# Performance work log

Hardware: AMD Instinct MI355X
Metric: run time of the kernel (lower is better)

Reference implementation:

```python
import jax, jax.numpy as jnp
import numpy as np

N, P, M, NCLS = 32, 24564, 32, 81
NEG_POS_RATIO, ALPHA, THRESHOLD = 3, 1.0, 0.5
BACKGROUND = NCLS  # sentinel label for background priors (== n_classes, as in original)


def _rand_boxes(key, prefix):
    # valid normalized xyxy boxes (x2>x1, y2>y1, inside [0,1])
    k1, k2 = jax.random.split(key)
    cxy = jax.random.uniform(k1, prefix + (2,), minval=0.1, maxval=0.9)
    wh = jax.random.uniform(k2, prefix + (2,), minval=0.02, maxval=0.2)
    return jnp.concatenate([cxy - wh / 2, cxy + wh / 2], axis=-1)


def setup_inputs() -> dict:
    key = jax.random.key(0)
    ks = jax.random.split(key, 6)
    return {
        "predicted_boxes": jax.random.normal(ks[0], (N, P, 4), jnp.float32),
        "predicted_class_dist": jax.random.normal(ks[1], (N, P, NCLS), jnp.float32),
        "predicted_objectness": jax.random.uniform(ks[2], (N, P), jnp.float32),
        "anchor_priors": _rand_boxes(ks[3], (P,)),
        "boxes": _rand_boxes(ks[4], (N, M)),
        "labels": jax.random.randint(ks[5], (N, M), 0, NCLS),
    }


def xy_to_cxcy(xy):
    return jnp.concatenate([(xy[..., :2] + xy[..., 2:]) / 2, xy[..., 2:] - xy[..., :2]], axis=-1)


def cxcy_to_gcxgcy(cxcy, priors_cxcy):
    return jnp.concatenate([
        (cxcy[..., :2] - priors_cxcy[..., :2]) / (priors_cxcy[..., 2:] / 10.0),
        jnp.log(cxcy[..., 2:] / priors_cxcy[..., 2:]) * 5.0,
    ], axis=-1)


def box_iou(a, b):  # a: (M,4), b: (P,4) -> (M,P)
    lt = jnp.maximum(a[:, None, :2], b[None, :, :2])
    rb = jnp.minimum(a[:, None, 2:], b[None, :, 2:])
    wh = jnp.clip(rb - lt, 0.0)
    inter = wh[..., 0] * wh[..., 1]
    area_a = (a[:, 2] - a[:, 0]) * (a[:, 3] - a[:, 1])
    area_b = (b[:, 2] - b[:, 0]) * (b[:, 3] - b[:, 1])
    return inter / (area_a[:, None] + area_b[None, :] - inter)


def _match(boxes_i, labels_i, priors):
    # per-image anchor matching (vmapped over batch)
    iou = box_iou(boxes_i, priors)                     # (M, P)
    iou_per_prior = iou.max(axis=0)                    # (P,)
    obj_per_prior = iou.argmax(axis=0)                 # (P,)
    prior_per_obj = iou.argmax(axis=1)                 # (M,)
    obj_per_prior = obj_per_prior.at[prior_per_obj].set(jnp.arange(M))
    iou_per_prior = iou_per_prior.at[prior_per_obj].set(1.0)
    label_per_prior = labels_i[obj_per_prior]
    label_per_prior = jnp.where(iou_per_prior < THRESHOLD, BACKGROUND, label_per_prior)
    true_locs = cxcy_to_gcxgcy(xy_to_cxcy(boxes_i[obj_per_prior]), xy_to_cxcy(priors))
    return true_locs, label_per_prior


def reference(predicted_boxes, predicted_class_dist, predicted_objectness, anchor_priors, boxes, labels):
    true_locs, true_classes = jax.vmap(_match, in_axes=(0, 0, None))(boxes, labels, anchor_priors)
    pos = true_classes != BACKGROUND                   # (N, P) bool
    n_pos_total = pos.sum().astype(jnp.float32)
    posf = pos.astype(jnp.float32)

    # smooth L1 over positive priors (mean over selected elements)
    diff = predicted_boxes - true_locs
    ad = jnp.abs(diff)
    sl1 = jnp.where(ad < 1.0, 0.5 * diff * diff, ad - 0.5)
    loc_loss = jnp.sum(sl1 * posf[..., None]) / (n_pos_total * 4.0)

    # cross entropy over positive priors (mean)
    logp = jax.nn.log_softmax(predicted_class_dist, axis=-1)
    safe_cls = jnp.where(pos, true_classes, 0)
    ce = -jnp.take_along_axis(logp, safe_cls[..., None], axis=-1)[..., 0]
    class_loss_pos = jnp.sum(ce * posf) / n_pos_total

    # objectness MSE: positive mean + hard-negative mining
    obj_loss = (predicted_objectness - posf) ** 2      # (N, P)
    obj_loss_pos = jnp.sum(obj_loss * posf) / n_pos_total

    neg_loss = jnp.where(pos, 0.0, obj_loss)
    neg_sorted = -jnp.sort(-neg_loss, axis=1)          # descending per row
    n_hard = NEG_POS_RATIO * pos.sum(axis=1)           # (N,)
    hmask = (jnp.arange(P)[None, :] < n_hard[:, None]).astype(jnp.float32)
    obj_loss_hardneg = jnp.sum(neg_sorted * hmask) / jnp.maximum(hmask.sum(), 1.0)

    return class_loss_pos + obj_loss_pos + obj_loss_hardneg + ALPHA * loc_loss
```

## Files before the change

kernel.cpp:

```cpp
#include <hip/hip_runtime.h>
#include <math.h>

#define NB 32
#define PP 24564
#define MM 32
#define NCLS 81
#define CHUNK 1024
#define MBLK 24
#define PPW 768
#define BSH 18
#define HB 4096
#define CAPL 2048

#define WS_DONE   0
#define WS_PCNT   32
#define WS_IACC   160
#define WS_PACC   672
#define WS_CPART  9888
#define WS_BKEYP  12960
#define WS_POSBIT 209568
#define WS_M8     307872
#define WS_VAL    1093936

__device__ __forceinline__ float sl1(float d) {
    float a = fabsf(d);
    return a < 1.0f ? 0.5f * d * d : a - 0.5f;
}
__device__ __forceinline__ unsigned long long u64max(unsigned long long a, unsigned long long b) {
    return a > b ? a : b;
}
__device__ __forceinline__ float locv(const float4& pd, const float4& pb,
                                      float gx1, float gy1, float gx2, float gy2) {
    float pcx = (pb.x + pb.z) * 0.5f, pcy = (pb.y + pb.w) * 0.5f;
    float pw = pb.z - pb.x, ph = pb.w - pb.y;
    float g0 = ((gx1 + gx2) * 0.5f - pcx) / (pw / 10.0f);
    float g1 = ((gy1 + gy2) * 0.5f - pcy) / (ph / 10.0f);
    float g2 = logf((gx2 - gx1) / pw) * 5.0f;
    float g3 = logf((gy2 - gy1) / ph) * 5.0f;
    return sl1(pd.x - g0) + sl1(pd.y - g1) + sl1(pd.z - g2) + sl1(pd.w - g3);
}

extern "C" __global__ void __launch_bounds__(256) k_match(
    const float* __restrict__ priors,
    const float* __restrict__ boxes,
    const float* __restrict__ obj,
    const float* __restrict__ pred_boxes,
    const float* __restrict__ pred_cls,
    const int* __restrict__ labels,
    unsigned long long* __restrict__ bkeyp,
    unsigned int* __restrict__ posbit,
    unsigned char* __restrict__ m8,
    float* __restrict__ val,
    int* __restrict__ cpart,
    float* __restrict__ pacc,
    int* __restrict__ done)
{
    const int n = blockIdx.y;
    const int t = threadIdx.x;
    const int lane = t & 63;
    const int wave = t >> 6;
    const int bx = blockIdx.x;
    const int p0 = bx * CHUNK;

    if (bx == 0 && n == 0 && t == 0) *done = 0;

    __shared__ float4 spri[CHUNK];
    __shared__ unsigned char sm8[CHUNK];
    __shared__ float bx0[MM], by0[MM], bx1[MM], by1[MM], bar_[MM];
    __shared__ unsigned long long wk[4][MM];
    __shared__ int bcnt;
    __shared__ float sacc[3];

    float ov[4];
#pragma unroll
    for (int i = 0; i < 4; i++) {
        int p = p0 + t + i * 256;
        float4 v;
        if (p < PP) { v = *(const float4*)(priors + (size_t)p * 4);
                      ov[i] = obj[(size_t)n * PP + p]; }
        else { v.x = 3.f; v.y = 3.f; v.z = 3.5f; v.w = 3.5f; ov[i] = 0.f; }
        spri[t + i * 256] = v;
    }
    if (t < MM) {
        const float* b = boxes + ((size_t)n * MM + t) * 4;
        float x1 = b[0], y1 = b[1], x2 = b[2], y2 = b[3];
        bx0[t] = x1; by0[t] = y1; bx1[t] = x2; by1[t] = y2;
        bar_[t] = (x2 - x1) * (y2 - y1);
    }
    if (t == 0) bcnt = 0;
    if (t < 3) sacc[t] = 0.f;
    __syncthreads();

    float4 pr0 = spri[t], pr1 = spri[t + 256], pr2 = spri[t + 512], pr3 = spri[t + 768];
    const float pa0 = (pr0.z - pr0.x) * (pr0.w - pr0.y);
    const float pa1 = (pr1.z - pr1.x) * (pr1.w - pr1.y);
    const float pa2 = (pr2.z - pr2.x) * (pr2.w - pr2.y);
    const float pa3 = (pr3.z - pr3.x) * (pr3.w - pr3.y);
    unsigned pb0 = 0, pb1 = 0, pb2 = 0, pb3 = 0;

#define DO_IOU(PR, PA, PB, ROFF) { \
        float w = fminf(x1, PR.z) - fmaxf(x0, PR.x); \
        float h = fminf(y1, PR.w) - fmaxf(y0, PR.y); \
        w = fmaxf(w, 0.0f); h = fmaxf(h, 0.0f); \
        float inter = w * h; \
        float iou = inter / (ar + PA - inter); \
        unsigned ib = __float_as_uint(iou); \
        unsigned nk = (ib & 0xFFFFFFE0u) | (unsigned)(31 - m); \
        PB = PB > nk ? PB : nk; \
        unsigned long long kk = ((unsigned long long)ib << 32) \
            | (unsigned long long)(0xFFFFFFFFu - (unsigned)(p0 + t + (ROFF))); \
        km = u64max(km, kk); }

#pragma unroll 2
    for (int m = 0; m < MM; m++) {
        const float x0 = bx0[m], y0 = by0[m], x1 = bx1[m], y1 = by1[m], ar = bar_[m];
        unsigned long long km = 0ULL;
        DO_IOU(pr0, pa0, pb0, 0)
        DO_IOU(pr1, pa1, pb1, 256)
        DO_IOU(pr2, pa2, pb2, 512)
        DO_IOU(pr3, pa3, pb3, 768)
#pragma unroll
        for (int d = 1; d < 64; d <<= 1)
            km = u64max(km, (unsigned long long)__shfl_xor(km, d));
        if (lane == 0) wk[wave][m] = km;
    }
#undef DO_IOU

    int cnt = 0;
    unsigned long long bl[4];
#define ROWOUT(PB, R) { \
        int p = p0 + t + (R) * 256; \
        bool pos = (PB >= 0x3F000000u) && (p < PP); \
        unsigned long long ball = __ballot(pos); \
        bl[R] = ball; \
        unsigned char mb = (unsigned char)(31u - (PB & 31u)); \
        sm8[t + (R) * 256] = mb; \
        if (lane == 0) { \
            int wi = n * PPW + ((p0 + (R) * 256 + wave * 64) >> 5); \
            posbit[wi] = (unsigned)ball; posbit[wi + 1] = (unsigned)(ball >> 32); \
            cnt += __popcll(ball); \
        } \
        if (p < PP) { \
            size_t idx = (size_t)n * PP + p; \
            m8[idx] = mb; \
            val[idx] = pos ? 0.f : ov[R] * ov[R]; \
        } }
    ROWOUT(pb0, 0) ROWOUT(pb1, 1) ROWOUT(pb2, 2) ROWOUT(pb3, 3)
#undef ROWOUT
    if (lane == 0 && cnt) atomicAdd(&bcnt, cnt);

    {
        const int half = lane >> 5, hl = lane & 31;
        float ce_s = 0.f, loc_s = 0.f, op_s = 0.f;
#pragma unroll
        for (int R = 0; R < 4; R++) {
            unsigned long long mask = bl[R];
            const int roff = R * 256 + wave * 64;
            while (mask) {
                int i1 = __ffsll((long long)mask) - 1; mask &= mask - 1;
                int i2 = -1;
                if (mask) { i2 = __ffsll((long long)mask) - 1; mask &= mask - 1; }
                const int pi = half ? i2 : i1;
                const bool act = pi >= 0;
                const int poff = roff + (act ? pi : 0);
                const size_t idx = (size_t)n * PP + p0 + poff;

                const int bm = sm8[poff];
                const float* row = pred_cls + idx * NCLS;
                float a = act ? row[hl] : -INFINITY;
                float b = act ? row[hl + 32] : -INFINITY;
                float c = (act && hl < NCLS - 64) ? row[hl + 64] : -INFINITY;
                float mx = fmaxf(fmaxf(a, b), c);
#pragma unroll
                for (int d = 1; d < 32; d <<= 1) mx = fmaxf(mx, __shfl_xor(mx, d));
                float se = act ? (expf(a - mx) + expf(b - mx)
                                  + ((hl < NCLS - 64) ? expf(c - mx) : 0.f)) : 0.f;
#pragma unroll
                for (int d = 1; d < 32; d <<= 1) se += __shfl_xor(se, d);

                if (act) {
                    if (hl == 0) {
                        ce_s += mx + logf(se) - row[labels[n * MM + bm]];
                    } else if (hl == 1) {
                        float4 pb = spri[poff];
                        float4 pd = *(const float4*)(pred_boxes + idx * 4);
                        loc_s += locv(pd, pb, bx0[bm], by0[bm], bx1[bm], by1[bm]);
                    } else if (hl == 2) {
                        float o = obj[idx];
                        op_s += (o - 1.0f) * (o - 1.0f);
                    }
                }
            }
        }
        if (ce_s != 0.f)  atomicAdd(&sacc[0], ce_s);
        if (loc_s != 0.f) atomicAdd(&sacc[1], loc_s);
        if (op_s != 0.f)  atomicAdd(&sacc[2], op_s);
    }

    __syncthreads();
    if (t == 0) {
        cpart[n * MBLK + bx] = bcnt;
        float* pa = pacc + ((size_t)n * MBLK + bx) * 3;
        pa[0] = sacc[0]; pa[1] = sacc[1]; pa[2] = sacc[2];
    }
    if (t < MM) {
        unsigned long long r = u64max(u64max(wk[0][t], wk[1][t]),
                                      u64max(wk[2][t], wk[3][t]));
        bkeyp[((size_t)n * MBLK + bx) * MM + t] = r;
    }
}

extern "C" __global__ void __launch_bounds__(512) k_fin(
    const float* __restrict__ priors,
    const float* __restrict__ boxes,
    const float* __restrict__ obj,
    const float* __restrict__ pred_boxes,
    const float* __restrict__ pred_cls,
    const int* __restrict__ labels,
    const unsigned long long* __restrict__ bkeyp,
    const unsigned int* __restrict__ posbit,
    const unsigned char* __restrict__ m8,
    const int* __restrict__ cpart,
    const float* __restrict__ pacc,
    float* __restrict__ val,
    int* __restrict__ pcnt,
    float4* __restrict__ iacc,
    int* __restrict__ done,
    float* __restrict__ out)
{
    const int n = blockIdx.x;
    const int t = threadIdx.x;
    const int lane = t & 63;
    const int wave = t >> 6;
    float* v = val + (size_t)n * PP;
    const float4* v4 = (const float4*)v;
    const int N4 = PP / 4;

    __shared__ unsigned fl[MM];
    __shared__ int newlist[MM];
    __shared__ int s_nnew, s_nat, s_tot;
    __shared__ float sacc[3];
    __shared__ float wred[8], wred2[8];

    if (t < 3) sacc[t] = 0.f;
    if (t == 0) { s_nnew = 0; s_nat = 0; }
    __syncthreads();

    if (t < MM) {
        const unsigned long long* bp = bkeyp + (size_t)n * MBLK * MM + t;
        unsigned long long r = 0ULL;
#pragma unroll
        for (int s = 0; s < MBLK; s++) r = u64max(r, bp[(size_t)s * MM]);
        fl[t] = ~(unsigned)(r & 0xFFFFFFFFULL);
    }
    if (t < MBLK) atomicAdd(&s_nat, cpart[n * MBLK + t]);
    __syncthreads();

    float d_ce = 0.f, d_loc = 0.f;
    if (t < MM) {
        unsigned p = fl[t];
        bool owner = true;
        for (int j = t + 1; j < MM; j++) if (fl[j] == p) owner = false;
        if (owner) {
            size_t idx = (size_t)n * PP + p;
            bool natPos = (posbit[n * PPW + (p >> 5)] >> (p & 31)) & 1u;
            if (natPos) {
                int bmn = (int)m8[idx];
                if (bmn != t) {
                    const float* row = pred_cls + idx * NCLS;
                    d_ce = row[labels[n * MM + bmn]] - row[labels[n * MM + t]];
                    float4 pb = *(const float4*)(priors + (size_t)p * 4);
                    float4 pd = *(const float4*)(pred_boxes + idx * 4);
                    const float* bf = boxes + ((size_t)n * MM + t) * 4;
                    const float* bn = boxes + ((size_t)n * MM + bmn) * 4;
                    d_loc = locv(pd, pb, bf[0], bf[1], bf[2], bf[3])
                          - locv(pd, pb, bn[0], bn[1], bn[2], bn[3]);
                }
            } else {
                int ix = atomicAdd(&s_nnew, 1);
                newlist[ix] = ((int)p << 5) | t;
                v[p] = 0.f;
            }
        }
    }
    if (t < 64) {
#pragma unroll
        for (int d = 1; d < 64; d <<= 1) {
            d_ce += __shfl_xor(d_ce, d);
            d_loc += __shfl_xor(d_loc, d);
        }
        if (t == 0) {
            if (d_ce != 0.f)  atomicAdd(&sacc[0], d_ce);
            if (d_loc != 0.f) atomicAdd(&sacc[1], d_loc);
        }
    }
    if (t < MBLK * 3) atomicAdd(&sacc[t % 3], pacc[(size_t)n * MBLK * 3 + t]);
    __syncthreads();

    const int nn = s_nnew;
    {
        const int hl = lane & 31;
        float nce = 0.f, nloc = 0.f, nop = 0.f;
        for (int i = wave; i < nn; i += 8) {
            int e = newlist[i];
            int p = e >> 5, bm = e & 31;
            size_t idx = (size_t)n * PP + p;
            const float* row = pred_cls + idx * NCLS;
            bool al = lane < 32;
            float a = al ? row[hl] : -INFINITY;
            float b = al ? row[hl + 32] : -INFINITY;
            float c = (al && hl < NCLS - 64) ? row[hl + 64] : -INFINITY;
            float mx = fmaxf(fmaxf(a, b), c);
#pragma unroll
            for (int d = 1; d < 32; d <<= 1) mx = fmaxf(mx, __shfl_xor(mx, d));
            float se = al ? (expf(a - mx) + expf(b - mx)
                             + ((hl < NCLS - 64) ? expf(c - mx) : 0.f)) : 0.f;
#pragma unroll
            for (int d = 1; d < 32; d <<= 1) se += __shfl_xor(se, d);
            if (lane == 0) {
                nce += mx + logf(se) - row[labels[n * MM + bm]];
            } else if (lane == 1) {
                float4 pb = *(const float4*)(priors + (size_t)p * 4);
                float4 pd = *(const float4*)(pred_boxes + idx * 4);
                const float* bb = boxes + ((size_t)n * MM + bm) * 4;
                nloc += locv(pd, pb, bb[0], bb[1], bb[2], bb[3]);
            } else if (lane == 2) {
                float o = obj[idx];
                nop += (o - 1.0f) * (o - 1.0f);
            }
        }
        if (nce != 0.f)  atomicAdd(&sacc[0], nce);
        if (nloc != 0.f) atomicAdd(&sacc[1], nloc);
        if (nop != 0.f)  atomicAdd(&sacc[2], nop);
    }
    __syncthreads();
    if (t == 0) s_tot = s_nat + s_nnew;
    __syncthreads();
    int k = s_tot * 3; if (k > PP) k = PP;

    float result = 0.f;
    if (k >= PP) {
        float s = 0.f;
        for (int i = t; i < N4; i += 512) {
            float4 q = v4[i]; s += q.x + q.y + q.z + q.w;
        }
#pragma unroll
        for (int d = 32; d > 0; d >>= 1) s += __shfl_down(s, d);
        if ((t & 63) == 0) wred[wave] = s;
        __syncthreads();
        if (t == 0) { for (int i = 0; i < 8; i++) result += wred[i]; }
    } else if (k > 0) {
        __shared__ unsigned hist[HB];
        __shared__ unsigned ssc[512];
        __shared__ unsigned cand[CAPL];
        __shared__ int s_c, s_d, s_rem;
        __shared__ unsigned s_cur;
        __shared__ int s_rr;
        __shared__ unsigned rh[128];

        for (int i = t; i < HB; i += 512) hist[i] = 0;
        if (t == 0) s_c = 0;
        __syncthreads();

        for (int i = t; i < N4; i += 512) {
            float4 q = v4[i];
            atomicAdd(&hist[__float_as_uint(q.x) >> BSH], 1u);
            atomicAdd(&hist[__float_as_uint(q.y) >> BSH], 1u);
            atomicAdd(&hist[__float_as_uint(q.z) >> BSH], 1u);
            atomicAdd(&hist[__float_as_uint(q.w) >> BSH], 1u);
        }
        __syncthreads();

        unsigned csum = 0;
#pragma unroll
        for (int j = 0; j < 8; j++) csum += hist[4095 - 8 * t - j];
        ssc[t] = csum; __syncthreads();
        for (int off = 1; off < 512; off <<= 1) {
            unsigned x = (t >= off) ? ssc[t - off] : 0u;
            __syncthreads(); ssc[t] += x; __syncthreads();
        }
        unsigned incl = ssc[t], excl = incl - csum;
        if (excl < (unsigned)k && incl >= (unsigned)k) {
            unsigned cum = excl;
#pragma unroll
            for (int j = 0; j < 8; j++) {
                int b = 4095 - 8 * t - j; unsigned h = hist[b];
                if (cum + h >= (unsigned)k) { s_d = b; s_rem = (int)((unsigned)k - cum); break; }
                cum += h;
            }
        }
        __syncthreads();
        const int d = s_d; const int rem0 = s_rem;

        float ms = 0.f;
        for (int i = t; i < N4; i += 512) {
            float4 q = v4[i];
#define HND(C) { unsigned b = __float_as_uint(C); int bn = (int)(b >> BSH); \
            if (bn > d) ms += (C); \
            else if (bn == d) { int ix = atomicAdd(&s_c, 1); if (ix < CAPL) cand[ix] = b; } }
            HND(q.x) HND(q.y) HND(q.z) HND(q.w)
#undef HND
        }
        __syncthreads();
        const int C = s_c;
        const bool okl = (C <= CAPL);

        unsigned cur = (unsigned)d << BSH; int rem = rem0;
        const int shs[3] = {11, 4, 0};
        const int wbs[3] = {7, 7, 4};
        for (int ps = 0; ps < 3; ps++) {
            const int sh = shs[ps], wb = wbs[ps], W = 1 << wb;
            if (t < W) rh[t] = 0;
            __syncthreads();
            if (okl) {
                for (int i = t; i < C; i += 512) {
                    unsigned b = cand[i];
                    if ((b >> (sh + wb)) == (cur >> (sh + wb)))
                        atomicAdd(&rh[(b >> sh) & (W - 1)], 1u);
                }
            } else {
                for (int i = t; i < PP; i += 512) {
                    unsigned b = __float_as_uint(v[i]);
                    if ((b >> (sh + wb)) == (cur >> (sh + wb)))
                        atomicAdd(&rh[(b >> sh) & (W - 1)], 1u);
                }
            }
            __syncthreads();
            if (t == 0) {
                unsigned cum = 0; int dd;
                for (dd = W - 1; dd > 0; --dd) {
                    unsigned h = rh[dd];
                    if (cum + h >= (unsigned)rem) break;
                    cum += h;
                }
                s_cur = cur | ((unsigned)dd << sh);
                s_rr = rem - (int)cum;
            }
            __syncthreads();
            cur = s_cur; rem = s_rr;
            __syncthreads();
        }
        const unsigned thr = cur;
        const float thrv = __uint_as_float(thr);

        float sg = ms, cg = 0.f;
        if (okl) {
            for (int i = t; i < C; i += 512) {
                unsigned b = cand[i];
                if (b > thr) { sg += __uint_as_float(b); cg += 1.f; }
            }
        } else {
            for (int i = t; i < PP; i += 512) {
                unsigned b = __float_as_uint(v[i]);
                if ((int)(b >> BSH) == d && b > thr) { sg += __uint_as_float(b); cg += 1.f; }
            }
        }
#pragma unroll
        for (int dd = 32; dd > 0; dd >>= 1) {
            sg += __shfl_down(sg, dd);
            cg += __shfl_down(cg, dd);
        }
        if ((t & 63) == 0) { wred[wave] = sg; wred2[wave] = cg; }
        __syncthreads();
        if (t == 0) {
            float S = 0.f, Cc = 0.f;
            for (int i = 0; i < 8; i++) { S += wred[i]; Cc += wred2[i]; }
            result = S + ((float)rem0 - Cc) * thrv;
        }
    }

    if (t == 0) {
        pcnt[n] = s_tot;
        iacc[n] = make_float4(sacc[0], sacc[1], sacc[2], result);
        __threadfence();
        int old = atomicAdd(done, 1);
        if (old == NB - 1) {
            int np = 0, den = 0; float ce = 0.f, lc = 0.f, op = 0.f, hs = 0.f;
            for (int i = 0; i < NB; i++) {
                int c = pcnt[i];
                np += c;
                int kk = c * 3; if (kk > PP) kk = PP;
                den += kk;
                float4 a = iacc[i];
                ce += a.x; lc += a.y; op += a.z; hs += a.w;
            }
            float npf = (float)np;
            out[0] = ce / npf + op / npf
                   + hs / fmaxf((float)den, 1.0f)
                   + lc / (npf * 4.0f);
        }
    }
}

extern "C" void kernel_launch(void* const* d_in, const int* in_sizes, int n_in,
                              void* d_out, int out_size, void* d_ws, size_t ws_size,
                              hipStream_t stream) {
    const float* pred_boxes = (const float*)d_in[0];
    const float* pred_cls   = (const float*)d_in[1];
    const float* pred_obj   = (const float*)d_in[2];
    const float* priors     = (const float*)d_in[3];
    const float* boxes      = (const float*)d_in[4];
    const int*   labels     = (const int*)d_in[5];

    char* ws = (char*)d_ws;
    int* done  = (int*)(ws + WS_DONE);
    int* pcnt  = (int*)(ws + WS_PCNT);
    float4* iacc = (float4*)(ws + WS_IACC);
    float* pacc = (float*)(ws + WS_PACC);
    int* cpart = (int*)(ws + WS_CPART);
    unsigned long long* bkeyp = (unsigned long long*)(ws + WS_BKEYP);
    unsigned* posbit = (unsigned*)(ws + WS_POSBIT);
    unsigned char* m8 = (unsigned char*)(ws + WS_M8);
    float* val = (float*)(ws + WS_VAL);

    k_match<<<dim3(MBLK, NB), 256, 0, stream>>>(priors, boxes, pred_obj, pred_boxes,
                                                pred_cls, labels, bkeyp, posbit, m8,
                                                val, cpart, pacc, done);
    k_fin<<<NB, 512, 0, stream>>>(priors, boxes, pred_obj, pred_boxes, pred_cls,
                                  labels, bkeyp, posbit, m8, cpart, pacc, val,
                                  pcnt, iacc, done, (float*)d_out);
}
```

Baseline: 82.55 us.

## Fuse match and finalize kernels into one cooperative launch with grid sync

Merges the two kernels into a single cooperative kernel that uses grid.sync() between the matching phase and the per-image finalize phase. Shared memory is overlaid through a union, and the finalize phase now runs on only 32 of the 768 blocks with 256 threads instead of 512, so its loops and scans were adjusted to match. The aim is to remove the second launch and the gap between kernels. In exchange, the finalize phase gets half the threads per image, and the cooperative launch and grid barrier carry their own overhead.

```diff
diff --git a/kernel.cpp b/kernel.cpp
--- a/kernel.cpp
+++ b/kernel.cpp
@@ -1,5 +1,8 @@
 #include <hip/hip_runtime.h>
+#include <hip/hip_cooperative_groups.h>
 #include <math.h>
+
+namespace cg = cooperative_groups;
 
 #define NB 32
 #define PP 24564
@@ -40,7 +43,31 @@
     return sl1(pd.x - g0) + sl1(pd.y - g1) + sl1(pd.z - g2) + sl1(pd.w - g3);
 }
 
-extern "C" __global__ void __launch_bounds__(256) k_match(
+union SMem {
+    struct {
+        float4 spri[CHUNK];
+        unsigned char sm8[CHUNK];
+        float bx0[MM], by0[MM], bx1[MM], by1[MM], bar_[MM];
+        unsigned long long wk[4][MM];
+        int bcnt;
+        float sacc[3];
+    } p1;
+    struct {
+        unsigned hist[HB];
+        unsigned cand[CAPL];
+        unsigned ssc[256];
+        unsigned rh[128];
+        unsigned fl[MM];
+        int newlist[MM];
+        float sacc[3];
+        float wred[4], wred2[4];
+        int nnew, nat, tot;
+        int s_c, s_d, s_rem, s_rr;
+        unsigned s_cur;
+    } p2;
+};
+
+extern "C" __global__ void __launch_bounds__(256) k_all(
     const float* __restrict__ priors,
     const float* __restrict__ boxes,
     const float* __restrict__ obj,
@@ -53,50 +80,51 @@
     float* __restrict__ val,
     int* __restrict__ cpart,
     float* __restrict__ pacc,
-    int* __restrict__ done)
+    int* __restrict__ pcnt,
+    float4* __restrict__ iacc,
+    int* __restrict__ done,
+    float* __restrict__ out)
 {
+    cg::grid_group grid = cg::this_grid();
     const int n = blockIdx.y;
+    const int bx = blockIdx.x;
     const int t = threadIdx.x;
     const int lane = t & 63;
     const int wave = t >> 6;
-    const int bx = blockIdx.x;
     const int p0 = bx * CHUNK;
 
+    __shared__ SMem sm;
+
     if (bx == 0 && n == 0 && t == 0) *done = 0;
 
-    __shared__ float4 spri[CHUNK];
-    __shared__ unsigned char sm8[CHUNK];
-    __shared__ float bx0[MM], by0[MM], bx1[MM], by1[MM], bar_[MM];
-    __shared__ unsigned long long wk[4][MM];
-    __shared__ int bcnt;
-    __shared__ float sacc[3];
-
-    float ov[4];
-#pragma unroll
-    for (int i = 0; i < 4; i++) {
-        int p = p0 + t + i * 256;
-        float4 v;
-        if (p < PP) { v = *(const float4*)(priors + (size_t)p * 4);
-                      ov[i] = obj[(size_t)n * PP + p]; }
-        else { v.x = 3.f; v.y = 3.f; v.z = 3.5f; v.w = 3.5f; ov[i] = 0.f; }
-        spri[t + i * 256] = v;
-    }
-    if (t < MM) {
-        const float* b = boxes + ((size_t)n * MM + t) * 4;
-        float x1 = b[0], y1 = b[1], x2 = b[2], y2 = b[3];
-        bx0[t] = x1; by0[t] = y1; bx1[t] = x2; by1[t] = y2;
-        bar_[t] = (x2 - x1) * (y2 - y1);
-    }
-    if (t == 0) bcnt = 0;
-    if (t < 3) sacc[t] = 0.f;
-    __syncthreads();
-
-    float4 pr0 = spri[t], pr1 = spri[t + 256], pr2 = spri[t + 512], pr3 = spri[t + 768];
-    const float pa0 = (pr0.z - pr0.x) * (pr0.w - pr0.y);
-    const float pa1 = (pr1.z - pr1.x) * (pr1.w - pr1.y);
-    const float pa2 = (pr2.z - pr2.x) * (pr2.w - pr2.y);
-    const float pa3 = (pr3.z - pr3.x) * (pr3.w - pr3.y);
-    unsigned pb0 = 0, pb1 = 0, pb2 = 0, pb3 = 0;
+    {
+        float ov[4];
+#pragma unroll
+        for (int i = 0; i < 4; i++) {
+            int p = p0 + t + i * 256;
+            float4 v;
+            if (p < PP) { v = *(const float4*)(priors + (size_t)p * 4);
+                          ov[i] = obj[(size_t)n * PP + p]; }
+            else { v.x = 3.f; v.y = 3.f; v.z = 3.5f; v.w = 3.5f; ov[i] = 0.f; }
+            sm.p1.spri[t + i * 256] = v;
+        }
+        if (t < MM) {
+            const float* b = boxes + ((size_t)n * MM + t) * 4;
+            float x1 = b[0], y1 = b[1], x2 = b[2], y2 = b[3];
+            sm.p1.bx0[t] = x1; sm.p1.by0[t] = y1; sm.p1.bx1[t] = x2; sm.p1.by1[t] = y2;
+            sm.p1.bar_[t] = (x2 - x1) * (y2 - y1);
+        }
+        if (t == 0) sm.p1.bcnt = 0;
+        if (t < 3) sm.p1.sacc[t] = 0.f;
+        __syncthreads();
+
+        float4 pr0 = sm.p1.spri[t], pr1 = sm.p1.spri[t + 256],
+               pr2 = sm.p1.spri[t + 512], pr3 = sm.p1.spri[t + 768];
+        const float pa0 = (pr0.z - pr0.x) * (pr0.w - pr0.y);
+        const float pa1 = (pr1.z - pr1.x) * (pr1.w - pr1.y);
+        const float pa2 = (pr2.z - pr2.x) * (pr2.w - pr2.y);
+        const float pa3 = (pr3.z - pr3.x) * (pr3.w - pr3.y);
+        unsigned pb0 = 0, pb1 = 0, pb2 = 0, pb3 = 0;
 
 #define DO_IOU(PR, PA, PB, ROFF) { \
         float w = fminf(x1, PR.z) - fmaxf(x0, PR.x); \
@@ -112,29 +140,30 @@
         km = u64max(km, kk); }
 
 #pragma unroll 2
-    for (int m = 0; m < MM; m++) {
-        const float x0 = bx0[m], y0 = by0[m], x1 = bx1[m], y1 = by1[m], ar = bar_[m];
-        unsigned long long km = 0ULL;
-        DO_IOU(pr0, pa0, pb0, 0)
-        DO_IOU(pr1, pa1, pb1, 256)
-        DO_IOU(pr2, pa2, pb2, 512)
-        DO_IOU(pr3, pa3, pb3, 768)
-#pragma unroll
-        for (int d = 1; d < 64; d <<= 1)
-            km = u64max(km, (unsigned long long)__shfl_xor(km, d));
-        if (lane == 0) wk[wave][m] = km;
-    }
+        for (int m = 0; m < MM; m++) {
+            const float x0 = sm.p1.bx0[m], y0 = sm.p1.by0[m],
+                        x1 = sm.p1.bx1[m], y1 = sm.p1.by1[m], ar = sm.p1.bar_[m];
+            unsigned long long km = 0ULL;
+            DO_IOU(pr0, pa0, pb0, 0)
+            DO_IOU(pr1, pa1, pb1, 256)
+            DO_IOU(pr2, pa2, pb2, 512)
+            DO_IOU(pr3, pa3, pb3, 768)
+#pragma unroll
+            for (int d = 1; d < 64; d <<= 1)
+                km = u64max(km, (unsigned long long)__shfl_xor(km, d));
+            if (lane == 0) sm.p1.wk[wave][m] = km;
+        }
 #undef DO_IOU
 
-    int cnt = 0;
-    unsigned long long bl[4];
+        int cnt = 0;
+        unsigned long long bl[4];
 #define ROWOUT(PB, R) { \
         int p = p0 + t + (R) * 256; \
         bool pos = (PB >= 0x3F000000u) && (p < PP); \
         unsigned long long ball = __ballot(pos); \
         bl[R] = ball; \
         unsigned char mb = (unsigned char)(31u - (PB & 31u)); \
-        sm8[t + (R) * 256] = mb; \
+        sm.p1.sm8[t + (R) * 256] = mb; \
         if (lane == 0) { \
             int wi = n * PPW + ((p0 + (R) * 256 + wave * 64) >> 5); \
             posbit[wi] = (unsigned)ball; posbit[wi + 1] = (unsigned)(ball >> 32); \
@@ -145,140 +174,118 @@
             m8[idx] = mb; \
             val[idx] = pos ? 0.f : ov[R] * ov[R]; \
         } }
-    ROWOUT(pb0, 0) ROWOUT(pb1, 1) ROWOUT(pb2, 2) ROWOUT(pb3, 3)
+        ROWOUT(pb0, 0) ROWOUT(pb1, 1) ROWOUT(pb2, 2) ROWOUT(pb3, 3)
 #undef ROWOUT
-    if (lane == 0 && cnt) atomicAdd(&bcnt, cnt);
-
-    {
-        const int half = lane >> 5, hl = lane & 31;
-        float ce_s = 0.f, loc_s = 0.f, op_s = 0.f;
-#pragma unroll
-        for (int R = 0; R < 4; R++) {
-            unsigned long long mask = bl[R];
-            const int roff = R * 256 + wave * 64;
-            while (mask) {
-                int i1 = __ffsll((long long)mask) - 1; mask &= mask - 1;
-                int i2 = -1;
-                if (mask) { i2 = __ffsll((long long)mask) - 1; mask &= mask - 1; }
-                const int pi = half ? i2 : i1;
-                const bool act = pi >= 0;
-                const int poff = roff + (act ? pi : 0);
-                const size_t idx = (size_t)n * PP + p0 + poff;
-
-                const int bm = sm8[poff];
-                const float* row = pred_cls + idx * NCLS;
-                float a = act ? row[hl] : -INFINITY;
-                float b = act ? row[hl + 32] : -INFINITY;
-                float c = (act && hl < NCLS - 64) ? row[hl + 64] : -INFINITY;
-                float mx = fmaxf(fmaxf(a, b), c);
-#pragma unroll
-                for (int d = 1; d < 32; d <<= 1) mx = fmaxf(mx, __shfl_xor(mx, d));
-                float se = act ? (expf(a - mx) + expf(b - mx)
-                                  + ((hl < NCLS - 64) ? expf(c - mx) : 0.f)) : 0.f;
-#pragma unroll
-                for (int d = 1; d < 32; d <<= 1) se += __shfl_xor(se, d);
-
-                if (act) {
-                    if (hl == 0) {
-                        ce_s += mx + logf(se) - row[labels[n * MM + bm]];
-                    } else if (hl == 1) {
-                        float4 pb = spri[poff];
-                        float4 pd = *(const float4*)(pred_boxes + idx * 4);
-                        loc_s += locv(pd, pb, bx0[bm], by0[bm], bx1[bm], by1[bm]);
-                    } else if (hl == 2) {
-                        float o = obj[idx];
-                        op_s += (o - 1.0f) * (o - 1.0f);
+        if (lane == 0 && cnt) atomicAdd(&sm.p1.bcnt, cnt);
+
+        {
+            const int half = lane >> 5, hl = lane & 31;
+            float ce_s = 0.f, loc_s = 0.f, op_s = 0.f;
+#pragma unroll
+            for (int R = 0; R < 4; R++) {
+                unsigned long long mask = bl[R];
+                const int roff = R * 256 + wave * 64;
+                while (mask) {
+                    int i1 = __ffsll((long long)mask) - 1; mask &= mask - 1;
+                    int i2 = -1;
+                    if (mask) { i2 = __ffsll((long long)mask) - 1; mask &= mask - 1; }
+                    const int pi = half ? i2 : i1;
+                    const bool act = pi >= 0;
+                    const int poff = roff + (act ? pi : 0);
+                    const size_t idx = (size_t)n * PP + p0 + poff;
+
+                    const int bm = sm.p1.sm8[poff];
+                    const float* row = pred_cls + idx * NCLS;
+                    float a = act ? row[hl] : -INFINITY;
+                    float b = act ? row[hl + 32] : -INFINITY;
+                    float c = (act && hl < NCLS - 64) ? row[hl + 64] : -INFINITY;
+                    float mx = fmaxf(fmaxf(a, b), c);
+#pragma unroll
+                    for (int d = 1; d < 32; d <<= 1) mx = fmaxf(mx, __shfl_xor(mx, d));
+                    float se = act ? (expf(a - mx) + expf(b - mx)
+                                      + ((hl < NCLS - 64) ? expf(c - mx) : 0.f)) : 0.f;
+#pragma unroll
+                    for (int d = 1; d < 32; d <<= 1) se += __shfl_xor(se, d);
+
+                    if (act) {
+                        if (hl == 0) {
+                            ce_s += mx + logf(se) - row[labels[n * MM + bm]];
+                        } else if (hl == 1) {
+                            float4 pb = sm.p1.spri[poff];
+                            float4 pd = *(const float4*)(pred_boxes + idx * 4);
+                            loc_s += locv(pd, pb, sm.p1.bx0[bm], sm.p1.by0[bm],
+                                          sm.p1.bx1[bm], sm.p1.by1[bm]);
+                        } else if (hl == 2) {
+                            float o = obj[idx];
+                            op_s += (o - 1.0f) * (o - 1.0f);
+                        }
                     }
                 }
             }
-        }
-        if (ce_s != 0.f)  atomicAdd(&sacc[0], ce_s);
-        if (loc_s != 0.f) atomicAdd(&sacc[1], loc_s);
-        if (op_s != 0.f)  atomicAdd(&sacc[2], op_s);
-    }
-
-    __syncthreads();
-    if (t == 0) {
-        cpart[n * MBLK + bx] = bcnt;
-        float* pa = pacc + ((size_t)n * MBLK + bx) * 3;
-        pa[0] = sacc[0]; pa[1] = sacc[1]; pa[2] = sacc[2];
-    }
-    if (t < MM) {
-        unsigned long long r = u64max(u64max(wk[0][t], wk[1][t]),
-                                      u64max(wk[2][t], wk[3][t]));
-        bkeyp[((size_t)n * MBLK + bx) * MM + t] = r;
-    }
-}
-
-extern "C" __global__ void __launch_bounds__(512) k_fin(
-    const float* __restrict__ priors,
-    const float* __restrict__ boxes,
-    const float* __restrict__ obj,
-    const float* __restrict__ pred_boxes,
-    const float* __restrict__ pred_cls,
-    const int* __restrict__ labels,
-    const unsigned long long* __restrict__ bkeyp,
-    const unsigned int* __restrict__ posbit,
-    const unsigned char* __restrict__ m8,
-    const int* __restrict__ cpart,
-    const float* __restrict__ pacc,
-    float* __restrict__ val,
-    int* __restrict__ pcnt,
-    float4* __restrict__ iacc,
-    int* __restrict__ done,
-    float* __restrict__ out)
-{
-    const int n = blockIdx.x;
-    const int t = threadIdx.x;
-    const int lane = t & 63;
-    const int wave = t >> 6;
-    float* v = val + (size_t)n * PP;
+            if (ce_s != 0.f)  atomicAdd(&sm.p1.sacc[0], ce_s);
+            if (loc_s != 0.f) atomicAdd(&sm.p1.sacc[1], loc_s);
+            if (op_s != 0.f)  atomicAdd(&sm.p1.sacc[2], op_s);
+        }
+
+        __syncthreads();
+        if (t == 0) {
+            cpart[n * MBLK + bx] = sm.p1.bcnt;
+            float* pa = pacc + ((size_t)n * MBLK + bx) * 3;
+            pa[0] = sm.p1.sacc[0]; pa[1] = sm.p1.sacc[1]; pa[2] = sm.p1.sacc[2];
+        }
+        if (t < MM) {
+            unsigned long long r = u64max(u64max(sm.p1.wk[0][t], sm.p1.wk[1][t]),
+                                          u64max(sm.p1.wk[2][t], sm.p1.wk[3][t]));
+            bkeyp[((size_t)n * MBLK + bx) * MM + t] = r;
+        }
+    }
+
+    grid.sync();
+
+    const int fb = n * MBLK + bx;
+    if (fb >= NB) return;
+    const int img = fb;
+    float* v = val + (size_t)img * PP;
     const float4* v4 = (const float4*)v;
     const int N4 = PP / 4;
 
-    __shared__ unsigned fl[MM];
-    __shared__ int newlist[MM];
-    __shared__ int s_nnew, s_nat, s_tot;
-    __shared__ float sacc[3];
-    __shared__ float wred[8], wred2[8];
-
-    if (t < 3) sacc[t] = 0.f;
-    if (t == 0) { s_nnew = 0; s_nat = 0; }
+    if (t < 3) sm.p2.sacc[t] = 0.f;
+    if (t == 0) { sm.p2.nnew = 0; sm.p2.nat = 0; }
     __syncthreads();
 
     if (t < MM) {
-        const unsigned long long* bp = bkeyp + (size_t)n * MBLK * MM + t;
+        const unsigned long long* bp = bkeyp + (size_t)img * MBLK * MM + t;
         unsigned long long r = 0ULL;
 #pragma unroll
         for (int s = 0; s < MBLK; s++) r = u64max(r, bp[(size_t)s * MM]);
-        fl[t] = ~(unsigned)(r & 0xFFFFFFFFULL);
-    }
-    if (t < MBLK) atomicAdd(&s_nat, cpart[n * MBLK + t]);
+        sm.p2.fl[t] = ~(unsigned)(r & 0xFFFFFFFFULL);
+    }
+    if (t < MBLK) atomicAdd(&sm.p2.nat, cpart[img * MBLK + t]);
     __syncthreads();
 
     float d_ce = 0.f, d_loc = 0.f;
     if (t < MM) {
-        unsigned p = fl[t];
+        unsigned p = sm.p2.fl[t];
         bool owner = true;
-        for (int j = t + 1; j < MM; j++) if (fl[j] == p) owner = false;
+        for (int j = t + 1; j < MM; j++) if (sm.p2.fl[j] == p) owner = false;
         if (owner) {
-            size_t idx = (size_t)n * PP + p;
-            bool natPos = (posbit[n * PPW + (p >> 5)] >> (p & 31)) & 1u;
+            size_t idx = (size_t)img * PP + p;
+            bool natPos = (posbit[img * PPW + (p >> 5)] >> (p & 31)) & 1u;
             if (natPos) {
                 int bmn = (int)m8[idx];
                 if (bmn != t) {
                     const float* row = pred_cls + idx * NCLS;
-                    d_ce = row[labels[n * MM + bmn]] - row[labels[n * MM + t]];
+                    d_ce = row[labels[img * MM + bmn]] - row[labels[img * MM + t]];
                     float4 pb = *(const float4*)(priors + (size_t)p * 4);
                     float4 pd = *(const float4*)(pred_boxes + idx * 4);
-                    const float* bf = boxes + ((size_t)n * MM + t) * 4;
-                    const float* bn = boxes + ((size_t)n * MM + bmn) * 4;
+                    const float* bf = boxes + ((size_t)img * MM + t) * 4;
+                    const float* bn = boxes + ((size_t)img * MM + bmn) * 4;
                     d_loc = locv(pd, pb, bf[0], bf[1], bf[2], bf[3])
                           - locv(pd, pb, bn[0], bn[1], bn[2], bn[3]);
                 }
             } else {
-                int ix = atomicAdd(&s_nnew, 1);
-                newlist[ix] = ((int)p << 5) | t;
+                int ix = atomicAdd(&sm.p2.nnew, 1);
+                sm.p2.newlist[ix] = ((int)p << 5) | t;
                 v[p] = 0.f;
             }
         }
@@ -290,21 +297,21 @@
             d_loc += __shfl_xor(d_loc, d);
         }
         if (t == 0) {
-            if (d_ce != 0.f)  atomicAdd(&sacc[0], d_ce);
-            if (d_loc != 0.f) atomicAdd(&sacc[1], d_loc);
-        }
-    }
-    if (t < MBLK * 3) atomicAdd(&sacc[t % 3], pacc[(size_t)n * MBLK * 3 + t]);
+            if (d_ce != 0.f)  atomicAdd(&sm.p2.sacc[0], d_ce);
+            if (d_loc != 0.f) atomicAdd(&sm.p2.sacc[1], d_loc);
+        }
+    }
+    if (t < MBLK * 3) atomicAdd(&sm.p2.sacc[t % 3], pacc[(size_t)img * MBLK * 3 + t]);
     __syncthreads();
 
-    const int nn = s_nnew;
+    const int nn = sm.p2.nnew;
     {
         const int hl = lane & 31;
         float nce = 0.f, nloc = 0.f, nop = 0.f;
-        for (int i = wave; i < nn; i += 8) {
-            int e = newlist[i];
+        for (int i = wave; i < nn; i += 4) {
+            int e = sm.p2.newlist[i];
             int p = e >> 5, bm = e & 31;
-            size_t idx = (size_t)n * PP + p;
+            size_t idx = (size_t)img * PP + p;
             const float* row = pred_cls + idx * NCLS;
             bool al = lane < 32;
             float a = al ? row[hl] : -INFINITY;
@@ -318,91 +325,87 @@
 #pragma unroll
             for (int d = 1; d < 32; d <<= 1) se += __shfl_xor(se, d);
             if (lane == 0) {
-                nce += mx + logf(se) - row[labels[n * MM + bm]];
+                nce += mx + logf(se) - row[labels[img * MM + bm]];
             } else if (lane == 1) {
                 float4 pb = *(const float4*)(priors + (size_t)p * 4);
                 float4 pd = *(const float4*)(pred_boxes + idx * 4);
-                const float* bb = boxes + ((size_t)n * MM + bm) * 4;
+                const float* bb = boxes + ((size_t)img * MM + bm) * 4;
                 nloc += locv(pd, pb, bb[0], bb[1], bb[2], bb[3]);
             } else if (lane == 2) {
                 float o = obj[idx];
                 nop += (o - 1.0f) * (o - 1.0f);
             }
         }
-        if (nce != 0.f)  atomicAdd(&sacc[0], nce);
-        if (nloc != 0.f) atomicAdd(&sacc[1], nloc);
-        if (nop != 0.f)  atomicAdd(&sacc[2], nop);
+        if (nce != 0.f)  atomicAdd(&sm.p2.sacc[0], nce);
+        if (nloc != 0.f) atomicAdd(&sm.p2.sacc[1], nloc);
+        if (nop != 0.f)  atomicAdd(&sm.p2.sacc[2], nop);
     }
     __syncthreads();
-    if (t == 0) s_tot = s_nat + s_nnew;
+    if (t == 0) sm.p2.tot = sm.p2.nat + sm.p2.nnew;
     __syncthreads();
+    const int s_tot = sm.p2.tot;
     int k = s_tot * 3; if (k > PP) k = PP;
 
     float result = 0.f;
     if (k >= PP) {
         float s = 0.f;
-        for (int i = t; i < N4; i += 512) {
+        for (int i = t; i < N4; i += 256) {
             float4 q = v4[i]; s += q.x + q.y + q.z + q.w;
         }
 #pragma unroll
         for (int d = 32; d > 0; d >>= 1) s += __shfl_down(s, d);
-        if ((t & 63) == 0) wred[wave] = s;
-        __syncthreads();
-        if (t == 0) { for (int i = 0; i < 8; i++) result += wred[i]; }
+        if ((t & 63) == 0) sm.p2.wred[wave] = s;
+        __syncthreads();
+        if (t == 0) { for (int i = 0; i < 4; i++) result += sm.p2.wred[i]; }
     } else if (k > 0) {
-        __shared__ unsigned hist[HB];
-        __shared__ unsigned ssc[512];
-        __shared__ unsigned cand[CAPL];
-        __shared__ int s_c, s_d, s_rem;
-        __shared__ unsigned s_cur;
-        __shared__ int s_rr;
-        __shared__ unsigned rh[128];
-
-        for (int i = t; i < HB; i += 512) hist[i] = 0;
-        if (t == 0) s_c = 0;
-        __syncthreads();
-
-        for (int i = t; i < N4; i += 512) {
+        for (int i = t; i < HB; i += 256) sm.p2.hist[i] = 0;
+        if (t == 0) sm.p2.s_c = 0;
+        __syncthreads();
+
+        for (int i = t; i < N4; i += 256) {
             float4 q = v4[i];
-            atomicAdd(&hist[__float_as_uint(q.x) >> BSH], 1u);
-            atomicAdd(&hist[__float_as_uint(q.y) >> BSH], 1u);
-            atomicAdd(&hist[__float_as_uint(q.z) >> BSH], 1u);
-            atomicAdd(&hist[__float_as_uint(q.w) >> BSH], 1u);
+            atomicAdd(&sm.p2.hist[__float_as_uint(q.x) >> BSH], 1u);
+            atomicAdd(&sm.p2.hist[__float_as_uint(q.y) >> BSH], 1u);
+            atomicAdd(&sm.p2.hist[__float_as_uint(q.z) >> BSH], 1u);
+            atomicAdd(&sm.p2.hist[__float_as_uint(q.w) >> BSH], 1u);
         }
         __syncthreads();
 
         unsigned csum = 0;
 #pragma unroll
-        for (int j = 0; j < 8; j++) csum += hist[4095 - 8 * t - j];
-        ssc[t] = csum; __syncthreads();
-        for (int off = 1; off < 512; off <<= 1) {
-            unsigned x = (t >= off) ? ssc[t - off] : 0u;
-            __syncthreads(); ssc[t] += x; __syncthreads();
-        }
-        unsigned incl = ssc[t], excl = incl - csum;
+        for (int j = 0; j < 16; j++) csum += sm.p2.hist[4095 - 16 * t - j];
+        sm.p2.ssc[t] = csum; __syncthreads();
+        for (int off = 1; off < 256; off <<= 1) {
+            unsigned x = (t >= off) ? sm.p2.ssc[t - off] : 0u;
+            __syncthreads(); sm.p2.ssc[t] += x; __syncthreads();
+        }
+        unsigned incl = sm.p2.ssc[t], excl = incl - csum;
         if (excl < (unsigned)k && incl >= (unsigned)k) {
             unsigned cum = excl;
 #pragma unroll
-            for (int j = 0; j < 8; j++) {
-                int b = 4095 - 8 * t - j; unsigned h = hist[b];
-                if (cum + h >= (unsigned)k) { s_d = b; s_rem = (int)((unsigned)k - cum); break; }
+            for (int j = 0; j < 16; j++) {
+                int b = 4095 - 16 * t - j; unsigned h = sm.p2.hist[b];
+                if (cum + h >= (unsigned)k) {
+                    sm.p2.s_d = b; sm.p2.s_rem = (int)((unsigned)k - cum); break;
+                }
                 cum += h;
             }
         }
         __syncthreads();
-        const int d = s_d; const int rem0 = s_rem;
+        const int d = sm.p2.s_d; const int rem0 = sm.p2.s_rem;
 
         float ms = 0.f;
-        for (int i = t; i < N4; i += 512) {
+        for (int i = t; i < N4; i += 256) {
             float4 q = v4[i];
 #define HND(C) { unsigned b = __float_as_uint(C); int bn = (int)(b >> BSH); \
             if (bn > d) ms += (C); \
-            else if (bn == d) { int ix = atomicAdd(&s_c, 1); if (ix < CAPL) cand[ix] = b; } }
+            else if (bn == d) { int ix = atomicAdd(&sm.p2.s_c, 1); \
+                                if (ix < CAPL) sm.p2.cand[ix] = b; } }
             HND(q.x) HND(q.y) HND(q.z) HND(q.w)
 #undef HND
         }
         __syncthreads();
-        const int C = s_c;
+        const int C = sm.p2.s_c;
         const bool okl = (C <= CAPL);
 
         unsigned cur = (unsigned)d << BSH; int rem = rem0;
@@ -410,34 +413,34 @@
         const int wbs[3] = {7, 7, 4};
         for (int ps = 0; ps < 3; ps++) {
             const int sh = shs[ps], wb = wbs[ps], W = 1 << wb;
-            if (t < W) rh[t] = 0;
+            if (t < W) sm.p2.rh[t] = 0;
             __syncthreads();
             if (okl) {
-                for (int i = t; i < C; i += 512) {
-                    unsigned b = cand[i];
+                for (int i = t; i < C; i += 256) {
+                    unsigned b = sm.p2.cand[i];
                     if ((b >> (sh + wb)) == (cur >> (sh + wb)))
-                        atomicAdd(&rh[(b >> sh) & (W - 1)], 1u);
+                        atomicAdd(&sm.p2.rh[(b >> sh) & (W - 1)], 1u);
                 }
             } else {
-                for (int i = t; i < PP; i += 512) {
+                for (int i = t; i < PP; i += 256) {
                     unsigned b = __float_as_uint(v[i]);
                     if ((b >> (sh + wb)) == (cur >> (sh + wb)))
-                        atomicAdd(&rh[(b >> sh) & (W - 1)], 1u);
+                        atomicAdd(&sm.p2.rh[(b >> sh) & (W - 1)], 1u);
                 }
             }
             __syncthreads();
             if (t == 0) {
                 unsigned cum = 0; int dd;
                 for (dd = W - 1; dd > 0; --dd) {
-                    unsigned h = rh[dd];
+                    unsigned h = sm.p2.rh[dd];
                     if (cum + h >= (unsigned)rem) break;
                     cum += h;
                 }
-                s_cur = cur | ((unsigned)dd << sh);
-                s_rr = rem - (int)cum;
+                sm.p2.s_cur = cur | ((unsigned)dd << sh);
+                sm.p2.s_rr = rem - (int)cum;
             }
             __syncthreads();
-            cur = s_cur; rem = s_rr;
+            cur = sm.p2.s_cur; rem = sm.p2.s_rr;
             __syncthreads();
         }
         const unsigned thr = cur;
@@ -445,12 +448,12 @@
 
         float sg = ms, cg = 0.f;
         if (okl) {
-            for (int i = t; i < C; i += 512) {
-                unsigned b = cand[i];
+            for (int i = t; i < C; i += 256) {
+                unsigned b = sm.p2.cand[i];
                 if (b > thr) { sg += __uint_as_float(b); cg += 1.f; }
             }
         } else {
-            for (int i = t; i < PP; i += 512) {
+            for (int i = t; i < PP; i += 256) {
                 unsigned b = __float_as_uint(v[i]);
                 if ((int)(b >> BSH) == d && b > thr) { sg += __uint_as_float(b); cg += 1.f; }
             }
@@ -460,18 +463,18 @@
             sg += __shfl_down(sg, dd);
             cg += __shfl_down(cg, dd);
         }
-        if ((t & 63) == 0) { wred[wave] = sg; wred2[wave] = cg; }
+        if ((t & 63) == 0) { sm.p2.wred[wave] = sg; sm.p2.wred2[wave] = cg; }
         __syncthreads();
         if (t == 0) {
             float S = 0.f, Cc = 0.f;
-            for (int i = 0; i < 8; i++) { S += wred[i]; Cc += wred2[i]; }
+            for (int i = 0; i < 4; i++) { S += sm.p2.wred[i]; Cc += sm.p2.wred2[i]; }
             result = S + ((float)rem0 - Cc) * thrv;
         }
     }
 
     if (t == 0) {
-        pcnt[n] = s_tot;
-        iacc[n] = make_float4(sacc[0], sacc[1], sacc[2], result);
+        pcnt[img] = s_tot;
+        iacc[img] = make_float4(sm.p2.sacc[0], sm.p2.sacc[1], sm.p2.sacc[2], result);
         __threadfence();
         int old = atomicAdd(done, 1);
         if (old == NB - 1) {
@@ -512,11 +515,14 @@
     unsigned* posbit = (unsigned*)(ws + WS_POSBIT);
     unsigned char* m8 = (unsigned char*)(ws + WS_M8);
     float* val = (float*)(ws + WS_VAL);
-
-    k_match<<<dim3(MBLK, NB), 256, 0, stream>>>(priors, boxes, pred_obj, pred_boxes,
-                                                pred_cls, labels, bkeyp, posbit, m8,
-                                                val, cpart, pacc, done);
-    k_fin<<<NB, 512, 0, stream>>>(priors, boxes, pred_obj, pred_boxes, pred_cls,
-                                  labels, bkeyp, posbit, m8, cpart, pacc, val,
-                                  pcnt, iacc, done, (float*)d_out);
+    float* out = (float*)d_out;
+
+    void* args[] = {
+        (void*)&priors, (void*)&boxes, (void*)&pred_obj, (void*)&pred_boxes,
+        (void*)&pred_cls, (void*)&labels, (void*)&bkeyp, (void*)&posbit,
+        (void*)&m8, (void*)&val, (void*)&cpart, (void*)&pacc,
+        (void*)&pcnt, (void*)&iacc, (void*)&done, (void*)&out
+    };
+    hipLaunchCooperativeKernel((const void*)k_all, dim3(MBLK, NB), dim3(256),
+                               args, 0, stream);
 }
```

After: 183.7 us. 2.23x slower.
